# Kernel optimization log

Hardware: AMD Instinct MI355X
Metric: run time of the kernel (lower is better)

## Reference

```python
import jax, jax.numpy as jnp
import numpy as np

S, B, D, H = 2048, 32, 256, 4
EPS = 1e-5


def setup_inputs() -> dict:
    key = jax.random.key(0)
    ks = jax.random.split(key, 16)
    f32 = jnp.float32

    def w(k, shape, scale=0.05):
        return jax.random.normal(k, shape, dtype=f32) * scale

    return {
        "q": jax.random.normal(ks[0], (S, B, D), f32),
        "k": jax.random.normal(ks[1], (S, B, D), f32),
        "v": jax.random.normal(ks[2], (S, B, D), f32),
        # per-head q/k/v projections, stacked over heads [H, D, D]
        "wq": w(ks[3], (H, D, D)), "bq": jnp.zeros((H, D), f32),
        "wk": w(ks[4], (H, D, D)), "bk": jnp.zeros((H, D), f32),
        "wv": w(ks[5], (H, D, D)), "bv": jnp.zeros((H, D), f32),
        # linear_w[i] = BN -> ReLU -> Linear -> BN -> ReLU -> Linear
        "g1": jnp.ones((H, D), f32), "be1": jnp.zeros((H, D), f32),
        "wl1": w(ks[6], (H, D, D)), "bl1": jnp.zeros((H, D), f32),
        "g2": jnp.ones((H, D), f32), "be2": jnp.zeros((H, D), f32),
        "wl2": w(ks[7], (H, D, D)), "bl2": jnp.zeros((H, D), f32),
        # final MLP: [D*H -> D -> D -> D]
        "mw0": w(ks[8], (D, D * H)), "mb0": jnp.zeros((D,), f32),
        "mw1": w(ks[9], (D, D)), "mb1": jnp.zeros((D,), f32),
        "mw2": w(ks[10], (D, D)), "mb2": jnp.zeros((D,), f32),
    }


def _bn(x, gamma, beta):
    # BatchNorm1d in training mode on permuted [B, D, S] tensor == per-channel
    # normalization over (S, B) axes of the [S, B, D] tensor; biased variance.
    m = x.mean(axis=(0, 1))
    v = x.var(axis=(0, 1))
    return (x - m) * jax.lax.rsqrt(v + EPS) * gamma + beta


def _lin(x, W, b):
    return x @ W.T + b


def reference(q, k, v, wq, bq, wk, bk, wv, bv, g1, be1, wl1, bl1,
              g2, be2, wl2, bl2, mw0, mb0, mw1, mb1, mw2, mb2):
    H_ = wq.shape[0]
    xs = []
    for i in range(H_):
        # NOTE: original code reassigns q/k/v, so projections chain across heads
        q = _lin(q, wq[i], bq[i])
        k = _lin(k, wk[i], bk[i])
        v = _lin(v, wv[i], bv[i])
        w = k - q                                  # [S, B, D]
        w = jax.nn.relu(_bn(w, g1[i], be1[i]))
        w = _lin(w, wl1[i], bl1[i])
        w = jax.nn.relu(_bn(w, g2[i], be2[i]))
        w = _lin(w, wl2[i], bl2[i])
        w = jax.nn.softmax(w, axis=0)              # softmax over seq dim
        xs.append((w * v).sum(axis=0))             # [B, D]
    x = jnp.concatenate(xs, axis=-1)[None]         # [1, B, H*D]
    x = jax.nn.relu(_lin(x, mw0, mb0))
    x = jax.nn.relu(_lin(x, mw1, mb1))
    x = _lin(x, mw2, mb2)                          # [1, B, D]
    return x
```

## Files before the change

### kernel.cpp

```cpp
#include <hip/hip_runtime.h>
#include <hip/hip_bf16.h>


typedef short  s16x8 __attribute__((ext_vector_type(8)));
typedef float  f32x4 __attribute__((ext_vector_type(4)));
typedef unsigned short u16;

constexpr int NC = 16;

__device__ __forceinline__ float bu2f(u16 u) {
    union { unsigned int i; float f; } c; c.i = ((unsigned int)u) << 16; return c.f;
}
__device__ __forceinline__ float bs2f(short s) { return bu2f((u16)s); }
__device__ __forceinline__ u16 f2bu(float f) {
    union { float f; unsigned int i; } c; c.f = f;
    unsigned int u = c.i;
    u += 0x7fffu + ((u >> 16) & 1u);
    return (u16)(u >> 16);
}
__device__ __forceinline__ unsigned int pack2(float a, float b) {
    __hip_bfloat162 h = __float22bfloat162_rn(make_float2(a, b));
    union { __hip_bfloat162 h; unsigned int u; } c; c.h = h; return c.u;
}

__global__ __launch_bounds__(256) void detect_k(const unsigned int* __restrict__ qw,
                                                int* __restrict__ flag)
{
    __shared__ int cnt[256];
    const int t = threadIdx.x;
    int c = 0;
    for (int i = 0; i < 64; i++) {
        const unsigned int w = qw[t + i * 256];
        const unsigned int e = (w >> 7) & 0xFFu;
        c += (e >= 96u && e <= 141u) ? 1 : 0;
    }
    cnt[t] = c;
    __syncthreads();
    for (int s = 128; s > 0; s >>= 1) {
        if (t < s) cnt[t] += cnt[t + s];
        __syncthreads();
    }
    if (t == 0) *flag = (cnt[0] > 8192) ? 1 : 0;
}

__global__ __launch_bounds__(256) void wconv_k(
    const void* w0, const void* w1, const void* w2, const void* w3, const void* w4,
    const int* __restrict__ dflag, u16* __restrict__ dst)
{
    const void* srcs[5] = {w0, w1, w2, w3, w4};
    const int y    = blockIdx.y;
    const int head = blockIdx.x >> 5;
    const int cb   = blockIdx.x & 31;
    const int c    = cb * 256 + threadIdx.x;
    const int l    = c & 63;
    const int ntl  = (c >> 6) & 7;
    const int half = (c >> 9) & 1;
    const int kk   = c >> 10;
    const int n    = half * 128 + ntl * 16 + (l & 15);
    const int k    = kk * 32 + ((l >> 4) & 3) * 8;
    const size_t so = (size_t)head * 65536 + (size_t)n * 256 + k;
    u16* d = dst + (size_t)y * 262144 + (size_t)head * 65536 + (size_t)c * 8;
    if (*dflag == 0) {
        const float* sf = (const float*)srcs[y] + so;
        f32x4 a = *(const f32x4*)sf;
        f32x4 b = *(const f32x4*)(sf + 4);
        union { s16x8 v; unsigned int w[4]; } o;
        o.w[0] = pack2(a[0], a[1]); o.w[1] = pack2(a[2], a[3]);
        o.w[2] = pack2(b[0], b[1]); o.w[3] = pack2(b[2], b[3]);
        *(s16x8*)d = o.v;
    } else {
        *(s16x8*)d = *(const s16x8*)((const u16*)srcs[y] + so);
    }
}

template<int AM, bool EXTA, int STATS>
__device__ __forceinline__ void gemm_core(
    const u16* __restrict__ A, const float* __restrict__ Af,
    const u16* __restrict__ A2, const u16* __restrict__ Qd,
    const u16* __restrict__ Wb,
    const u16* __restrict__ bias16, const float* __restrict__ biasf,
    const u16* __restrict__ g16, const float* __restrict__ gf,
    const u16* __restrict__ be16, const float* __restrict__ bef,
    const float* __restrict__ statsIn, float* __restrict__ statsOut,
    const int f32in, u16* __restrict__ C, const int bx)
{
    __shared__ __align__(16) u16 smem[12288];
    __shared__ float sc_s[256], sh_s[256];
    __shared__ float red_s[256];
    u16* As = smem;
    u16* Bs = smem + 4096;

    const int tid   = threadIdx.x;
    const int work  = ((bx & 7) << 8) | (bx >> 3);
    const int tileN = work & 1;
    const int tileM = work >> 1;
    const int lane  = tid & 63;
    const int wave  = tid >> 6;
    const int wm    = wave & 1;
    const int wn    = wave >> 1;
    const int lrow  = lane & 15;
    const int quad  = lane >> 4;

    const long rowA = (long)tileM * 64;
    const int  rowB = tileN * 128;

    if constexpr (AM != 0) {
        const int c = tid;
        float s = 0.f, q = 0.f;
#pragma unroll
        for (int i = 0; i < NC; i++) {
            s += statsIn[i * 256 + c];
            q += statsIn[(NC + i) * 256 + c];
        }
        const float mean = s * (1.f / 65536.f);
        const float var  = q * (1.f / 65536.f) - mean * mean;
        const float rstd = rsqrtf(var + 1e-5f);
        const float gg = f32in ? gf[c] : bu2f(g16[c]);
        const float bb = f32in ? bef[c] : bu2f(be16[c]);
        sc_s[c] = rstd * gg;
        sh_s[c] = bb - mean * rstd * gg;
        __syncthreads();
    }

    f32x4 acc[2][4];
#pragma unroll
    for (int i = 0; i < 2; i++)
#pragma unroll
        for (int j = 0; j < 4; j++) acc[i][j] = (f32x4){0.f, 0.f, 0.f, 0.f};

    for (int s = 0; s < 4; s++) {
        if (s) __syncthreads();

#pragma unroll
        for (int j = 0; j < 4; j++) {
            const int cp = j * 256 + tid;
            const u16* src = Wb
                + (size_t)((2 * s + (cp >> 9)) * 2 + tileN) * 4096
                + (size_t)(cp & 511) * 8;
            __builtin_amdgcn_global_load_lds(
                (const __attribute__((address_space(1))) void*)src,
                (__attribute__((address_space(3))) void*)(Bs + cp * 8), 16, 0, 0);
        }

#pragma unroll
        for (int j = 0; j < 2; j++) {
            const int cp  = j * 256 + tid;
            const int kk  = cp >> 8;
            const int wmi = (cp >> 7) & 1;
            const int imi = (cp >> 6) & 1;
            const int l   = cp & 63;
            const long row = rowA + wmi * 32 + imi * 16 + (l & 15);
            const int  col = s * 64 + kk * 32 + ((l >> 4) & 3) * 8;
            const long off = row * 256 + col;
            if constexpr (AM == 0) {
                if (EXTA && f32in) {
                    const float* p = Af + off;
                    f32x4 a = *(const f32x4*)p;
                    f32x4 b = *(const f32x4*)(p + 4);
                    union { s16x8 v; unsigned int w[4]; } o;
                    o.w[0] = pack2(a[0], a[1]); o.w[1] = pack2(a[2], a[3]);
                    o.w[2] = pack2(b[0], b[1]); o.w[3] = pack2(b[2], b[3]);
                    *(s16x8*)(As + cp * 8) = o.v;
                } else {
                    __builtin_amdgcn_global_load_lds(
                        (const __attribute__((address_space(1))) void*)(A + off),
                        (__attribute__((address_space(3))) void*)(As + cp * 8), 16, 0, 0);
                }
            } else {
                s16x8 xv = *(const s16x8*)(A + off);
                s16x8 yv;
                if constexpr (AM == 1) yv = *(const s16x8*)(A2 + off);
                float d[8];
#pragma unroll
                for (int e = 0; e < 8; e++) {
                    float x = bs2f(xv[e]);
                    if constexpr (AM == 1) x -= bs2f(yv[e]);
                    d[e] = fmaxf(fmaf(x, sc_s[col + e], sh_s[col + e]), 0.f);
                }
                union { s16x8 v; unsigned int w[4]; } o;
                o.w[0] = pack2(d[0], d[1]); o.w[1] = pack2(d[2], d[3]);
                o.w[2] = pack2(d[4], d[5]); o.w[3] = pack2(d[6], d[7]);
                *(s16x8*)(As + cp * 8) = o.v;
            }
        }

        __syncthreads();

        s16x8 af[2][2], bf[2][4];
#pragma unroll
        for (int kk = 0; kk < 2; kk++) {
#pragma unroll
            for (int im = 0; im < 2; im++)
                af[kk][im] = *(const s16x8*)(As + (((kk * 2 + wm) * 2 + im) * 64 + lane) * 8);
#pragma unroll
            for (int in = 0; in < 4; in++)
                bf[kk][in] = *(const s16x8*)(Bs + ((kk * 8 + wn * 4 + in) * 64 + lane) * 8);
        }
#pragma unroll
        for (int kk = 0; kk < 2; kk++)
#pragma unroll
            for (int im = 0; im < 2; im++)
#pragma unroll
                for (int in = 0; in < 4; in++)
                    acc[im][in] = __builtin_amdgcn_mfma_f32_16x16x32_bf16(
                        af[kk][im], bf[kk][in], acc[im][in], 0, 0, 0);
    }

    __syncthreads();
    u16* Cs = smem;
#pragma unroll
    for (int in = 0; in < 4; in++) {
        const int col  = wn * 64 + in * 16 + lrow;
        const int gcol = rowB + col;
        const float bv = f32in ? biasf[gcol] : bu2f(bias16[gcol]);
#pragma unroll
        for (int im = 0; im < 2; im++) {
            const int r0 = wm * 32 + im * 16 + quad * 4;
#pragma unroll
            for (int e = 0; e < 4; e++)
                Cs[(r0 + e) * 128 + col] = f2bu(acc[im][in][e] + bv);
        }
    }
    __syncthreads();

    if constexpr (STATS != 0) {
        const int colL = tid & 127;
        const int half = tid >> 7;
        float s = 0.f, qs = 0.f;
#pragma unroll 4
        for (int r = half * 32; r < half * 32 + 32; r++) {
            float x = bu2f(Cs[r * 128 + colL]);
            if constexpr (STATS == 1) x -= bu2f(Qd[(rowA + r) * 256 + rowB + colL]);
            s += x; qs += x * x;
        }
        red_s[tid] = s;
        __syncthreads();
        float sTot = 0.f;
        if (tid < 128) sTot = red_s[tid] + red_s[tid + 128];
        __syncthreads();
        red_s[tid] = qs;
        __syncthreads();
        if (tid < 128) {
            const float qTot = red_s[tid] + red_s[tid + 128];
            const int copy = tileM & (NC - 1);
            atomicAdd(&statsOut[copy * 256 + rowB + colL], sTot);
            atomicAdd(&statsOut[(NC + copy) * 256 + rowB + colL], qTot);
        }
    }

#pragma unroll
    for (int it = 0; it < 4; it++) {
        const int r  = it * 16 + (tid >> 4);
        const int c8 = (tid & 15) * 8;
        *(s16x8*)(C + (rowA + r) * 256 + rowB + c8) = *(const s16x8*)(Cs + r * 128 + c8);
    }
}

template<int AM, bool EXTA, int STATS>
__global__ __launch_bounds__(256) void gemm_k(
    const u16* A, const float* Af, const u16* A2, const u16* Qd,
    const u16* Wb, const void* bias, const void* g, const void* be, int hoff,
    const float* statsIn, float* statsOut, const int* dflag, u16* C)
{
    const int f32in = (*dflag == 0);
    gemm_core<AM, EXTA, STATS>(A, Af, A2, Qd, Wb,
        (const u16*)bias + hoff, (const float*)bias + hoff,
        (const u16*)g + hoff,    (const float*)g + hoff,
        (const u16*)be + hoff,   (const float*)be + hoff,
        statsIn, statsOut, f32in, C, blockIdx.x);
}

template<bool EXTA>
__global__ __launch_bounds__(256) void proj2_k(
    const u16* A0, const float* A0f, const u16* W0, const void* b0, u16* C0,
    const u16* A1, const float* A1f, const u16* W1, const void* b1, u16* C1,
    int hoff, const int* dflag)
{
    const int f32in = (*dflag == 0);
    const int y = blockIdx.y;
    gemm_core<0, EXTA, 0>(
        y ? A1 : A0, y ? A1f : A0f, nullptr, nullptr, y ? W1 : W0,
        (const u16*)(y ? b1 : b0) + hoff, (const float*)(y ? b1 : b0) + hoff,
        nullptr, nullptr, nullptr, nullptr, nullptr, nullptr,
        f32in, y ? C1 : C0, blockIdx.x);
}

__global__ __launch_bounds__(256) void softmax_chunk_k(
    const u16* __restrict__ L, const u16* __restrict__ V,
    float* __restrict__ pm, float* __restrict__ pl, float* __restrict__ pa)
{
    const int d = threadIdx.x, b = blockIdx.x, ch = blockIdx.y;
    float m = -3.0e38f, l = 0.f, acc = 0.f;
    const long base = ((long)ch * 64 * 32 + b) * 256 + d;
    for (int si = 0; si < 64; si++) {
        const long idx = base + (long)si * 32 * 256;
        const float x = bu2f(L[idx]);
        const float v = bu2f(V[idx]);
        const float mn = fmaxf(m, x);
        const float c  = __expf(m - mn);
        const float e  = __expf(x - mn);
        l   = l * c + e;
        acc = acc * c + e * v;
        m = mn;
    }
    const int p = (ch * 32 + b) * 256 + d;
    pm[p] = m; pl[p] = l; pa[p] = acc;
}

__global__ __launch_bounds__(256) void softmax_merge_k(
    const float* __restrict__ pm, const float* __restrict__ pl,
    const float* __restrict__ pa, float* __restrict__ xcat, int head)
{
    const int d = threadIdx.x, b = blockIdx.x;
    float M = -3.0e38f, L = 0.f, A = 0.f;
    for (int ch = 0; ch < 32; ch++) {
        const int p = (ch * 32 + b) * 256 + d;
        const float m = pm[p], l = pl[p], a = pa[p];
        const float mn = fmaxf(M, m);
        const float c1 = __expf(M - mn), c2 = __expf(m - mn);
        L = L * c1 + l * c2;
        A = A * c1 + a * c2;
        M = mn;
    }
    xcat[b * 1024 + head * 256 + d] = A / L;
}

__global__ __launch_bounds__(256) void mlp_k(
    const float* __restrict__ xcat,
    const u16* __restrict__ mw0, const float* __restrict__ mw0f,
    const u16* __restrict__ mb0, const float* __restrict__ mb0f,
    const u16* __restrict__ mw1, const float* __restrict__ mw1f,
    const u16* __restrict__ mb1, const float* __restrict__ mb1f,
    const u16* __restrict__ mw2, const float* __restrict__ mw2f,
    const u16* __restrict__ mb2, const float* __restrict__ mb2f,
    const int* __restrict__ dflag,
    u16* __restrict__ out, float* __restrict__ outf)
{
    __shared__ float h0[1024];
    __shared__ float h1[256];
    __shared__ float h2[256];
    const int f32in = (*dflag == 0);
    const int j = threadIdx.x, b = blockIdx.x;
#pragma unroll
    for (int i = 0; i < 4; i++) h0[j + i * 256] = xcat[b * 1024 + j + i * 256];
    __syncthreads();

    float a0 = f32in ? mb0f[j] : bu2f(mb0[j]);
    if (f32in) {
        for (int k4 = 0; k4 < 256; k4++) {
            f32x4 wv = *(const f32x4*)(mw0f + j * 1024 + k4 * 4);
#pragma unroll
            for (int e = 0; e < 4; e++) a0 += h0[k4 * 4 + e] * wv[e];
        }
    } else {
        for (int k8 = 0; k8 < 128; k8++) {
            s16x8 wv = *(const s16x8*)(mw0 + j * 1024 + k8 * 8);
#pragma unroll
            for (int e = 0; e < 8; e++) a0 += h0[k8 * 8 + e] * bs2f(wv[e]);
        }
    }
    h1[j] = fmaxf(a0, 0.f);
    __syncthreads();

    float a1 = f32in ? mb1f[j] : bu2f(mb1[j]);
    if (f32in) {
        for (int k4 = 0; k4 < 64; k4++) {
            f32x4 wv = *(const f32x4*)(mw1f + j * 256 + k4 * 4);
#pragma unroll
            for (int e = 0; e < 4; e++) a1 += h1[k4 * 4 + e] * wv[e];
        }
    } else {
        for (int k8 = 0; k8 < 32; k8++) {
            s16x8 wv = *(const s16x8*)(mw1 + j * 256 + k8 * 8);
#pragma unroll
            for (int e = 0; e < 8; e++) a1 += h1[k8 * 8 + e] * bs2f(wv[e]);
        }
    }
    h2[j] = fmaxf(a1, 0.f);
    __syncthreads();

    float a2 = f32in ? mb2f[j] : bu2f(mb2[j]);
    if (f32in) {
        for (int k4 = 0; k4 < 64; k4++) {
            f32x4 wv = *(const f32x4*)(mw2f + j * 256 + k4 * 4);
#pragma unroll
            for (int e = 0; e < 4; e++) a2 += h2[k4 * 4 + e] * wv[e];
        }
    } else {
        for (int k8 = 0; k8 < 32; k8++) {
            s16x8 wv = *(const s16x8*)(mw2 + j * 256 + k8 * 8);
#pragma unroll
            for (int e = 0; e < 8; e++) a2 += h2[k8 * 8 + e] * bs2f(wv[e]);
        }
    }
    if (f32in) outf[b * 256 + j] = a2;
    else       out[b * 256 + j] = f2bu(a2);
}

extern "C" void kernel_launch(void* const* d_in, const int* in_sizes, int n_in,
                              void* d_out, int out_size, void* d_ws, size_t ws_size,
                              hipStream_t stream)
{
    const u16 *q16 = (const u16*)d_in[0], *k16 = (const u16*)d_in[1], *v16 = (const u16*)d_in[2];
    const float *qf = (const float*)d_in[0], *kf = (const float*)d_in[1], *vf = (const float*)d_in[2];

    const size_t TEN = 33554432ull;
    const size_t WBF_OFF = 2097152ull;
    const size_t BUF_OFF = 5242880ull;
    if (ws_size < BUF_OFF + 5 * TEN) return;

    char* ws = (char*)d_ws;
    int*   dflag = (int*)ws;
    float* fb    = (float*)ws;
    float* sums  = fb + 256;
    float* xcat  = sums + 8 * 2 * NC * 256;
    u16*   wbf   = (u16*)(ws + WBF_OFF);
    u16* buf[5];
    for (int i = 0; i < 5; i++) buf[i] = (u16*)(ws + BUF_OFF + (size_t)i * TEN);

    const int qsrc[4] = {-1, 0, 3, 1}, qdst[4] = {0, 3, 1, 4};
    const int ksrc[4] = {-1, 1, 4, 2}, kdst[4] = {1, 4, 2, 0};
    const int vsrc[4] = {-1, 2, 0, 3}, vdst[4] = {2, 0, 3, 1};
    const int x1i[4]  = {3, 1, 4, 2},  lgi[4]  = {4, 2, 0, 3};

    detect_k<<<dim3(1), dim3(256), 0, stream>>>((const unsigned int*)d_in[0], dflag);
    hipMemsetAsync(sums, 0, 8 * 2 * NC * 256 * sizeof(float), stream);
    wconv_k<<<dim3(128, 5), dim3(256), 0, stream>>>(
        d_in[3], d_in[5], d_in[7], d_in[11], d_in[15], dflag, wbf);

    for (int h = 0; h < 4; h++) {
        const u16* qi = h ? (const u16*)buf[qsrc[h]] : q16;
        const u16* ki = h ? (const u16*)buf[ksrc[h]] : k16;
        const u16* vi = h ? (const u16*)buf[vsrc[h]] : v16;
        u16* qo = buf[qdst[h]];
        u16* ko = buf[kdst[h]];
        u16* vo = buf[vdst[h]];
        u16* x1b = buf[x1i[h]];
        u16* lgb = buf[lgi[h]];
        const u16* Wq  = wbf + (0 * 4 + h) * 65536;
        const u16* Wk  = wbf + (1 * 4 + h) * 65536;
        const u16* Wv  = wbf + (2 * 4 + h) * 65536;
        const u16* Wl1 = wbf + (3 * 4 + h) * 65536;
        const u16* Wl2 = wbf + (4 * 4 + h) * 65536;
        float* st1 = sums + (h * 2 + 0) * 2 * NC * 256;
        float* st2 = sums + (h * 2 + 1) * 2 * NC * 256;
        float* parts = (float*)x1b;
        const int hoff = h * 256;

        if (h == 0)
            proj2_k<true><<<dim3(2048, 2), dim3(256), 0, stream>>>(
                q16, qf, Wq, d_in[4], qo, v16, vf, Wv, d_in[8], vo, hoff, dflag);
        else
            proj2_k<false><<<dim3(2048, 2), dim3(256), 0, stream>>>(
                qi, nullptr, Wq, d_in[4], qo, vi, nullptr, Wv, d_in[8], vo, hoff, dflag);

        if (h == 0)
            gemm_k<0, true, 1><<<dim3(2048), dim3(256), 0, stream>>>(
                k16, kf, nullptr, qo, Wk, d_in[6], d_in[6], d_in[6], hoff,
                nullptr, st1, dflag, ko);
        else
            gemm_k<0, false, 1><<<dim3(2048), dim3(256), 0, stream>>>(
                ki, nullptr, nullptr, qo, Wk, d_in[6], d_in[6], d_in[6], hoff,
                nullptr, st1, dflag, ko);

        gemm_k<1, false, 2><<<dim3(2048), dim3(256), 0, stream>>>(
            ko, nullptr, qo, nullptr, Wl1, d_in[12], d_in[9], d_in[10], hoff,
            st1, st2, dflag, x1b);

        gemm_k<2, false, 0><<<dim3(2048), dim3(256), 0, stream>>>(
            x1b, nullptr, nullptr, nullptr, Wl2, d_in[16], d_in[13], d_in[14], hoff,
            st2, nullptr, dflag, lgb);

        softmax_chunk_k<<<dim3(32, 32), dim3(256), 0, stream>>>(
            lgb, vo, parts, parts + 262144, parts + 524288);
        softmax_merge_k<<<dim3(32), dim3(256), 0, stream>>>(
            parts, parts + 262144, parts + 524288, xcat, h);
    }
    mlp_k<<<dim3(32), dim3(256), 0, stream>>>(
        xcat,
        (const u16*)d_in[17], (const float*)d_in[17],
        (const u16*)d_in[18], (const float*)d_in[18],
        (const u16*)d_in[19], (const float*)d_in[19],
        (const u16*)d_in[20], (const float*)d_in[20],
        (const u16*)d_in[21], (const float*)d_in[21],
        (const u16*)d_in[22], (const float*)d_in[22],
        dflag, (u16*)d_out, (float*)d_out);
}
```

Measured before the change: 858.2 us.

## Triple-buffer GEMM K-loop with async prefetch and explicit vmcnt waits

```diff
diff --git a/kernel.cpp b/kernel.cpp
--- a/kernel.cpp
+++ b/kernel.cpp
@@ -21,6 +21,17 @@
 __device__ __forceinline__ unsigned int pack2(float a, float b) {
     __hip_bfloat162 h = __float22bfloat162_rn(make_float2(a, b));
     union { __hip_bfloat162 h; unsigned int u; } c; c.h = h; return c.u;
+}
+
+__device__ __forceinline__ void wait_vm(int n) {
+    switch (n) {
+        case 0: asm volatile("s_waitcnt vmcnt(0)" ::: "memory"); break;
+        case 2: asm volatile("s_waitcnt vmcnt(2)" ::: "memory"); break;
+        case 3: asm volatile("s_waitcnt vmcnt(3)" ::: "memory"); break;
+        case 4: asm volatile("s_waitcnt vmcnt(4)" ::: "memory"); break;
+        default: asm volatile("s_waitcnt vmcnt(6)" ::: "memory"); break;
+    }
+    __builtin_amdgcn_sched_barrier(0);
 }
 
 __global__ __launch_bounds__(256) void detect_k(const unsigned int* __restrict__ qw,
@@ -84,11 +95,9 @@
     const float* __restrict__ statsIn, float* __restrict__ statsOut,
     const int f32in, u16* __restrict__ C, const int bx)
 {
-    __shared__ __align__(16) u16 smem[12288];
+    __shared__ __align__(16) u16 smem[18432];
     __shared__ float sc_s[256], sh_s[256];
     __shared__ float red_s[256];
-    u16* As = smem;
-    u16* Bs = smem + 4096;
 
     const int tid   = threadIdx.x;
     const int work  = ((bx & 7) << 8) | (bx >> 3);
@@ -122,88 +131,100 @@
         __syncthreads();
     }
 
-    f32x4 acc[2][4];
-#pragma unroll
-    for (int i = 0; i < 2; i++)
-#pragma unroll
-        for (int j = 0; j < 4; j++) acc[i][j] = (f32x4){0.f, 0.f, 0.f, 0.f};
-
-    for (int s = 0; s < 4; s++) {
-        if (s) __syncthreads();
-
-#pragma unroll
-        for (int j = 0; j < 4; j++) {
+    const int nst = (AM != 0 || (EXTA && f32in)) ? 2 : 3;
+
+    auto issueW = [&](int s, u16* Bs) {
+#pragma unroll
+        for (int j = 0; j < 2; j++) {
             const int cp = j * 256 + tid;
-            const u16* src = Wb
-                + (size_t)((2 * s + (cp >> 9)) * 2 + tileN) * 4096
-                + (size_t)(cp & 511) * 8;
+            const u16* src = Wb + ((size_t)s * 1024 + (size_t)tileN * 512 + cp) * 8;
             __builtin_amdgcn_global_load_lds(
                 (const __attribute__((address_space(1))) void*)src,
                 (__attribute__((address_space(3))) void*)(Bs + cp * 8), 16, 0, 0);
         }
-
-#pragma unroll
-        for (int j = 0; j < 2; j++) {
-            const int cp  = j * 256 + tid;
-            const int kk  = cp >> 8;
-            const int wmi = (cp >> 7) & 1;
-            const int imi = (cp >> 6) & 1;
-            const int l   = cp & 63;
-            const long row = rowA + wmi * 32 + imi * 16 + (l & 15);
-            const int  col = s * 64 + kk * 32 + ((l >> 4) & 3) * 8;
-            const long off = row * 256 + col;
-            if constexpr (AM == 0) {
-                if (EXTA && f32in) {
-                    const float* p = Af + off;
-                    f32x4 a = *(const f32x4*)p;
-                    f32x4 b = *(const f32x4*)(p + 4);
-                    union { s16x8 v; unsigned int w[4]; } o;
-                    o.w[0] = pack2(a[0], a[1]); o.w[1] = pack2(a[2], a[3]);
-                    o.w[2] = pack2(b[0], b[1]); o.w[3] = pack2(b[2], b[3]);
-                    *(s16x8*)(As + cp * 8) = o.v;
-                } else {
-                    __builtin_amdgcn_global_load_lds(
-                        (const __attribute__((address_space(1))) void*)(A + off),
-                        (__attribute__((address_space(3))) void*)(As + cp * 8), 16, 0, 0);
-                }
+    };
+
+    auto stage = [&](int s, int b) {
+        u16* As = smem + b * 6144;
+        u16* Bs = As + 2048;
+        const int cp = tid;
+        const int l  = cp & 63;
+        const long row = rowA + ((cp >> 7) & 1) * 32 + ((cp >> 6) & 1) * 16 + (l & 15);
+        const int  col = s * 32 + ((l >> 4) & 3) * 8;
+        const long off = row * 256 + col;
+        if constexpr (AM == 0) {
+            if (EXTA && f32in) {
+                const float* p = Af + off;
+                f32x4 a = *(const f32x4*)p;
+                f32x4 bb = *(const f32x4*)(p + 4);
+                union { s16x8 v; unsigned int w[4]; } o;
+                o.w[0] = pack2(a[0], a[1]); o.w[1] = pack2(a[2], a[3]);
+                o.w[2] = pack2(bb[0], bb[1]); o.w[3] = pack2(bb[2], bb[3]);
+                *(s16x8*)(As + cp * 8) = o.v;
+                __builtin_amdgcn_sched_barrier(0);
+                issueW(s, Bs);
             } else {
-                s16x8 xv = *(const s16x8*)(A + off);
-                s16x8 yv;
-                if constexpr (AM == 1) yv = *(const s16x8*)(A2 + off);
-                float d[8];
-#pragma unroll
-                for (int e = 0; e < 8; e++) {
-                    float x = bs2f(xv[e]);
-                    if constexpr (AM == 1) x -= bs2f(yv[e]);
-                    d[e] = fmaxf(fmaf(x, sc_s[col + e], sh_s[col + e]), 0.f);
-                }
-                union { s16x8 v; unsigned int w[4]; } o;
-                o.w[0] = pack2(d[0], d[1]); o.w[1] = pack2(d[2], d[3]);
-                o.w[2] = pack2(d[4], d[5]); o.w[3] = pack2(d[6], d[7]);
-                *(s16x8*)(As + cp * 8) = o.v;
+                issueW(s, Bs);
+                __builtin_amdgcn_global_load_lds(
+                    (const __attribute__((address_space(1))) void*)(A + off),
+                    (__attribute__((address_space(3))) void*)(As + cp * 8), 16, 0, 0);
             }
-        }
-
-        __syncthreads();
-
-        s16x8 af[2][2], bf[2][4];
-#pragma unroll
-        for (int kk = 0; kk < 2; kk++) {
+        } else {
+            s16x8 xv = *(const s16x8*)(A + off);
+            s16x8 yv;
+            if constexpr (AM == 1) yv = *(const s16x8*)(A2 + off);
+            float d[8];
+#pragma unroll
+            for (int e = 0; e < 8; e++) {
+                float x = bs2f(xv[e]);
+                if constexpr (AM == 1) x -= bs2f(yv[e]);
+                d[e] = fmaxf(fmaf(x, sc_s[col + e], sh_s[col + e]), 0.f);
+            }
+            union { s16x8 v; unsigned int w[4]; } o;
+            o.w[0] = pack2(d[0], d[1]); o.w[1] = pack2(d[2], d[3]);
+            o.w[2] = pack2(d[4], d[5]); o.w[3] = pack2(d[6], d[7]);
+            *(s16x8*)(As + cp * 8) = o.v;
+            __builtin_amdgcn_sched_barrier(0);
+            issueW(s, Bs);
+        }
+    };
+
+    f32x4 acc[2][4];
+#pragma unroll
+    for (int i = 0; i < 2; i++)
+#pragma unroll
+        for (int j = 0; j < 4; j++) acc[i][j] = (f32x4){0.f, 0.f, 0.f, 0.f};
+
+    stage(0, 0);
+    stage(1, 1);
+    for (int s = 0; s < 8; s++) {
+        const int b = s % 3;
+        if (s < 6) stage(s + 2, (s + 2) % 3);
+        const int grp = (s < 6) ? 2 : (s == 6 ? 1 : 0);
+        wait_vm(grp * nst);
+        __builtin_amdgcn_s_barrier();
+        __builtin_amdgcn_sched_barrier(0);
+        {
+            const u16* As = smem + b * 6144;
+            const u16* Bs = As + 2048;
+            s16x8 af[2], bf[4];
 #pragma unroll
             for (int im = 0; im < 2; im++)
-                af[kk][im] = *(const s16x8*)(As + (((kk * 2 + wm) * 2 + im) * 64 + lane) * 8);
+                af[im] = *(const s16x8*)(As + ((wm * 2 + im) * 64 + lane) * 8);
 #pragma unroll
             for (int in = 0; in < 4; in++)
-                bf[kk][in] = *(const s16x8*)(Bs + ((kk * 8 + wn * 4 + in) * 64 + lane) * 8);
-        }
-#pragma unroll
-        for (int kk = 0; kk < 2; kk++)
+                bf[in] = *(const s16x8*)(Bs + ((wn * 4 + in) * 64 + lane) * 8);
 #pragma unroll
             for (int im = 0; im < 2; im++)
 #pragma unroll
                 for (int in = 0; in < 4; in++)
                     acc[im][in] = __builtin_amdgcn_mfma_f32_16x16x32_bf16(
-                        af[kk][im], bf[kk][in], acc[im][in], 0, 0, 0);
+                        af[im], bf[in], acc[im][in], 0, 0, 0);
+        }
+        if (s < 7) {
+            __builtin_amdgcn_sched_barrier(0);
+            __builtin_amdgcn_s_barrier();
+        }
     }
 
     __syncthreads();
```

Result: no change. 868.1 us (+1.2%).
